# Kernel optimization log

Hardware: AMD Instinct MI355X
Metric: run time of the kernel (lower is better)

## Reference

```python
import jax, jax.numpy as jnp
import numpy as np

HEADS = 4
DIM_QK = 128
DIM_V = 128
FMAP = 32  # H = W = 32, L = 1024
DIM = 512
B = 16


def rel_to_abs(x):
    # x: [B, Nh, L, 2L-1] -> [B, Nh, L, L]
    b, nh, L, _ = x.shape
    x = jnp.pad(x, ((0, 0), (0, 0), (0, 0), (0, 1)))          # [B, Nh, L, 2L]
    flat = x.reshape(b, nh, L * 2 * L)
    flat = jnp.pad(flat, ((0, 0), (0, 0), (0, L - 1)))
    final = flat.reshape(b, nh, L + 1, 2 * L - 1)
    return final[:, :, :L, L - 1:]


def relative_logits_1d(q, rel_k):
    # q: [B, Nh, H, W, d], rel_k: [2W-1, d] -> [B, Nh, H, H, W, W]
    b, nh, h, w, _ = q.shape
    rl = jnp.einsum('bnhwd,md->bnhwm', q, rel_k)
    rl = rl.reshape(b, nh * h, w, 2 * w - 1)
    rl = rel_to_abs(rl)                                        # [B, Nh*H, W, W]
    rl = rl.reshape(b, nh, h, w, w)
    rl = jnp.broadcast_to(rl[:, :, :, None], (b, nh, h, h, w, w))
    return rl


def rel_pos_logits(q, rel_height, rel_width):
    # q: [B, Nh, L, d] with L = FMAP*FMAP -> [B, Nh, L, L]
    b, nh, L, d = q.shape
    h = w = FMAP
    q5 = q.reshape(b, nh, h, w, d)
    # width logits: 'b n x i y j -> b n (x y) (i j)'
    rw = relative_logits_1d(q5, rel_width)
    rw = rw.transpose(0, 1, 2, 4, 3, 5).reshape(b, nh, h * w, h * w)
    # height logits: transpose spatial, then 'b n x i y j -> b n (y x) (j i)'
    rh = relative_logits_1d(q5.transpose(0, 1, 3, 2, 4), rel_height)
    rh = rh.transpose(0, 1, 4, 2, 5, 3).reshape(b, nh, h * w, h * w)
    return rw + rh


def setup_inputs() -> dict:
    key = jax.random.key(0)
    k1, k2, k3, k4, k5 = jax.random.split(key, 5)
    scale = DIM_QK ** -0.5
    return {
        'featuremap': jax.random.normal(k1, (B, DIM, FMAP, FMAP), jnp.float32),
        'w_qk': jax.random.normal(k2, (2 * HEADS * DIM_QK, DIM), jnp.float32) * (DIM ** -0.5),
        'w_v': jax.random.normal(k3, (HEADS * DIM_V, DIM), jnp.float32) * (DIM ** -0.5),
        'rel_height': jax.random.normal(k4, (2 * FMAP - 1, DIM_QK), jnp.float32) * scale,
        'rel_width': jax.random.normal(k5, (2 * FMAP - 1, DIM_QK), jnp.float32) * scale,
    }


def reference(featuremap, w_qk, w_v, rel_height, rel_width):
    b, c, h, w = featuremap.shape
    L = h * w
    # 1x1 convs (no bias) == channel matmuls
    qk = jnp.einsum('bchw,oc->bohw', featuremap, w_qk)
    q, k = jnp.split(qk, 2, axis=1)
    v = jnp.einsum('bchw,oc->bohw', featuremap, w_v)

    def to_heads(x, d):
        # 'B (h d) H W -> B h (H W) d'
        return x.reshape(b, HEADS, d, L).transpose(0, 1, 3, 2)

    q = to_heads(q, DIM_QK) * (DIM_QK ** -0.5)
    k = to_heads(k, DIM_QK)
    v = to_heads(v, DIM_V)

    logits = jnp.einsum('bhxd,bhyd->bhxy', q, k)
    logits = logits + rel_pos_logits(q, rel_height, rel_width)
    weights = jax.nn.softmax(logits, axis=-1)
    attn = jnp.einsum('bhxy,bhyd->bhxd', weights, v)
    # 'B h (H W) d -> B (h d) H W'
    out = attn.transpose(0, 1, 3, 2).reshape(b, HEADS * DIM_V, h, w)
    return out
```

## Files before the change

### kernel.cpp

```cpp
#include <hip/hip_runtime.h>
#include <hip/hip_bf16.h>
#include <math.h>

typedef __bf16 bf16x8 __attribute__((ext_vector_type(8)));
typedef float f32x4 __attribute__((ext_vector_type(4)));

#define QSCALE_L2E (0.08838834764831845f * 1.4426950408889634f)

static __device__ __forceinline__ unsigned short bits_bf16(float v) {
  __hip_bfloat16 h = __float2bfloat16(v);
  return *reinterpret_cast<unsigned short*>(&h);
}

static __device__ __forceinline__ void gload16(const void* g, void* l) {
  __builtin_amdgcn_global_load_lds(
      (const __attribute__((address_space(1))) void*)g,
      (__attribute__((address_space(3))) void*)l, 16, 0, 0);
}

__global__ __launch_bounds__(256) void k_convw(const float* __restrict__ wqk,
                                               const float* __restrict__ wv,
                                               const float* __restrict__ relw,
                                               const float* __restrict__ relh,
                                               __hip_bfloat16* __restrict__ wall,
                                               __hip_bfloat16* __restrict__ relsb) {
  int i = blockIdx.x * 256 + threadIdx.x;
  if (i < 1536 * 512) {
    float v = (i < 1024 * 512) ? wqk[i] : wv[i - 1024 * 512];
    wall[i] = __float2bfloat16(v);
  } else {
    int j = i - 1536 * 512;
    int t = j >> 13, m = (j >> 7) & 63, d = j & 127;
    float v = (m < 63) ? (t ? relh[m * 128 + d] : relw[m * 128 + d]) : 0.f;
    relsb[j] = __float2bfloat16(v);
  }
}

__global__ __launch_bounds__(256) void k_tfm(const float* __restrict__ fm,
                                             __hip_bfloat16* __restrict__ fmt) {
  __shared__ float t[64][65];
  int lt = blockIdx.x, ct = blockIdx.y, b = blockIdx.z;
  int tid = threadIdx.x;
  const float* src = fm + ((size_t)b * 512 + ct * 64) * 1024 + lt * 64;
#pragma unroll
  for (int i = 0; i < 16; ++i) {
    int idx = i * 256 + tid;
    int r = idx >> 6, cl = idx & 63;
    t[r][cl] = src[(size_t)r * 1024 + cl];
  }
  __syncthreads();
  __hip_bfloat16* dst = fmt + ((size_t)b * 1024 + lt * 64) * 512 + ct * 64;
#pragma unroll
  for (int i = 0; i < 16; ++i) {
    int idx = i * 256 + tid;
    int r = idx >> 6, cc = idx & 63;
    dst[(size_t)r * 512 + cc] = __float2bfloat16(t[cc][r]);
  }
}

__global__ __launch_bounds__(256) void k_gemm(const __hip_bfloat16* __restrict__ fmt,
                                              const __hip_bfloat16* __restrict__ wall,
                                              __hip_bfloat16* __restrict__ Qb,
                                              __hip_bfloat16* __restrict__ Kb,
                                              __hip_bfloat16* __restrict__ Vt) {
  __shared__ char smem[32768];
  char* As = smem;
  char* Bs = smem + 16384;
  int bm = blockIdx.x, bn = blockIdx.y, b = blockIdx.z;
  int tid = threadIdx.x;
  int lane = tid & 63, wave = tid >> 6;
  int wr = wave >> 1, wc = wave & 1;
  int g = lane >> 4, ln = lane & 15;
  const char* Ag = (const char*)(fmt + ((size_t)b * 1024 + bm * 128) * 512);
  const char* Bg = (const char*)(wall + (size_t)bn * 128 * 512);

  int j3 = lane >> 3, j7 = lane & 7;
  int segsrc = ((j7 ^ j3) << 4);

  f32x4 acc[4][4] = {};
  for (int kb = 0; kb < 8; ++kb) {
#pragma unroll
    for (int i = 0; i < 4; ++i) {
      int R = (wave * 4 + i) * 8;
      size_t go = (size_t)(R + j3) * 1024 + (size_t)kb * 128 + segsrc;
      gload16(Ag + go, As + R * 128);
      gload16(Bg + go, Bs + R * 128);
    }
    __syncthreads();
#pragma unroll
    for (int ks = 0; ks < 2; ++ks) {
      int kcol = ks * 64 + (g << 4);
      bf16x8 af[4], bfr[4];
#pragma unroll
      for (int m = 0; m < 4; ++m) {
        int row = wr * 64 + m * 16 + ln;
        af[m] = *(const bf16x8*)(As + row * 128 + (kcol ^ ((ln & 7) << 4)));
      }
#pragma unroll
      for (int n = 0; n < 4; ++n) {
        int row = wc * 64 + n * 16 + ln;
        bfr[n] = *(const bf16x8*)(Bs + row * 128 + (kcol ^ ((ln & 7) << 4)));
      }
#pragma unroll
      for (int m = 0; m < 4; ++m)
#pragma unroll
        for (int n = 0; n < 4; ++n)
          acc[m][n] = __builtin_amdgcn_mfma_f32_16x16x32_bf16(af[m], bfr[n], acc[m][n], 0, 0, 0);
    }
    __syncthreads();
  }

  int otype = bn >> 2;
  int head = bn & 3;
  if (otype != 2) {
    float sc = (otype == 0) ? QSCALE_L2E : 1.0f;
#pragma unroll
    for (int m = 0; m < 4; ++m)
#pragma unroll
      for (int n = 0; n < 4; ++n) {
        int d = wc * 64 + n * 16 + ln;
#pragma unroll
        for (int r = 0; r < 4; ++r) {
          int l = wr * 64 + m * 16 + g * 4 + r;
          *(__hip_bfloat16*)(smem + l * 256 + ((d * 2) ^ ((l & 7) << 4))) =
              __float2bfloat16(acc[m][n][r] * sc);
        }
      }
    __syncthreads();
    __hip_bfloat16* dstb =
        (otype == 0 ? Qb : Kb) + (((size_t)(b * 4 + head) * 1024) + bm * 128) * 128;
#pragma unroll
    for (int i = 0; i < 8; ++i) {
      int idx = i * 256 + tid;
      int row = idx >> 4, c16 = idx & 15;
      uint4 v = *(const uint4*)(smem + row * 256 + ((c16 * 16) ^ ((row & 7) << 4)));
      *(uint4*)(dstb + (size_t)row * 128 + c16 * 8) = v;
    }
  } else {
#pragma unroll
    for (int m = 0; m < 4; ++m)
#pragma unroll
      for (int n = 0; n < 4; ++n) {
        int d = wc * 64 + n * 16 + ln;
        int lbase = wr * 64 + m * 16 + g * 4;
        ushort4 pk;
        pk.x = bits_bf16(acc[m][n][0]);
        pk.y = bits_bf16(acc[m][n][1]);
        pk.z = bits_bf16(acc[m][n][2]);
        pk.w = bits_bf16(acc[m][n][3]);
        *(ushort4*)(smem + d * 256 + ((lbase * 2) ^ ((d & 7) << 4))) = pk;
      }
    __syncthreads();
    __hip_bfloat16* dstb = Vt + ((size_t)(b * 4 + head) * 128) * 1024 + bm * 128;
#pragma unroll
    for (int i = 0; i < 8; ++i) {
      int idx = i * 256 + tid;
      int row = idx >> 4, c16 = idx & 15;
      uint4 v = *(const uint4*)(smem + row * 256 + ((c16 * 16) ^ ((row & 7) << 4)));
      *(uint4*)(dstb + (size_t)row * 1024 + c16 * 8) = v;
    }
  }
}

__global__ __launch_bounds__(256) void k_bias(const __hip_bfloat16* __restrict__ Qb,
                                              const __hip_bfloat16* __restrict__ relsb,
                                              float* __restrict__ QRW,
                                              float* __restrict__ QRH) {
  __shared__ char sh[32768];
  int bx = blockIdx.x, bh = blockIdx.y;
  int tid = threadIdx.x, lane = tid & 63, wave = tid >> 6;
  int g = lane >> 4, ln = lane & 15;
#pragma unroll
  for (int i = 0; i < 8; ++i) {
    int chunk = i * 256 + tid;
    int row = chunk >> 4, c16 = chunk & 15;
    *(uint4*)(sh + row * 256 + ((c16 * 16) ^ ((row & 7) << 4))) =
        *(const uint4*)(relsb + (size_t)row * 128 + c16 * 8);
  }
  __syncthreads();
  size_t bhL = (size_t)bh * 1024;
  int l0 = bx * 128 + wave * 32;
  const __hip_bfloat16* Qg = Qb + (bhL + l0) * 128;
  bf16x8 a[2][4];
#pragma unroll
  for (int lf = 0; lf < 2; ++lf)
#pragma unroll
    for (int ks = 0; ks < 4; ++ks)
      a[lf][ks] = *(const bf16x8*)(Qg + (size_t)(lf * 16 + ln) * 128 + ks * 32 + g * 8);
#pragma unroll
  for (int t = 0; t < 2; ++t) {
    float* dst = (t == 0 ? QRW : QRH) + (bhL + l0) * 64;
#pragma unroll
    for (int n = 0; n < 4; ++n) {
      f32x4 acc2[2] = {};
#pragma unroll
      for (int ks = 0; ks < 4; ++ks) {
        int mrow = n * 16 + ln;
        bf16x8 bf = *(const bf16x8*)(sh + t * 16384 + mrow * 256 +
                                     ((ks * 64 + g * 16) ^ ((mrow & 7) << 4)));
#pragma unroll
        for (int lf = 0; lf < 2; ++lf)
          acc2[lf] = __builtin_amdgcn_mfma_f32_16x16x32_bf16(a[lf][ks], bf, acc2[lf], 0, 0, 0);
      }
#pragma unroll
      for (int lf = 0; lf < 2; ++lf)
#pragma unroll
        for (int r = 0; r < 4; ++r)
          dst[(size_t)(lf * 16 + g * 4 + r) * 64 + n * 16 + ln] = acc2[lf][r];
    }
  }
}

__global__ __launch_bounds__(512, 2) void k_attn(const __hip_bfloat16* __restrict__ Qb,
                                                 const __hip_bfloat16* __restrict__ Kb,
                                                 const __hip_bfloat16* __restrict__ Vt,
                                                 const float* __restrict__ QRW,
                                                 const float* __restrict__ QRH,
                                                 float* __restrict__ out) {
  extern __shared__ char smem[];
  float* hb_s = (float*)smem;
  char* kbuf = smem + 40960;
  char* vbuf = smem + 40960 + 32768;
  char* pt = smem + 40960 + 65536;

  int bh = blockIdx.x, qt = blockIdx.y;
  int b = bh >> 2, h = bh & 3;
  int tid = threadIdx.x, lane = tid & 63, wave = tid >> 6;
  int g = lane >> 4, ln = lane & 15;
  int q0 = qt * 256;
  size_t bhL = (size_t)bh * 1024;

#pragma unroll
  for (int i = 0; i < 5; ++i) {
    int c = i * 512 + tid;
    if (c < 2304) {
      int row = c / 9, j = c % 9;
      int s0 = (31 - ((q0 + row) >> 5)) & ~3;
      *(uint4*)(hb_s + row * 40 + j * 4) =
          *(const uint4*)(QRH + (bhL + q0 + row) * 64 + s0 + j * 4);
    }
  }

  bf16x8 qa[2][4];
  float wb[2][2][4];
  int qloc[2], hbase[2];
#pragma unroll
  for (int u = 0; u < 2; ++u) {
    qloc[u] = wave * 32 + u * 16 + ln;
    int qg = q0 + qloc[u];
    int cx = qg & 31, rx = qg >> 5;
    hbase[u] = (31 - rx) & 3;
    const __hip_bfloat16* qrow = Qb + (bhL + qg) * 128;
#pragma unroll
    for (int ks = 0; ks < 4; ++ks)
      qa[u][ks] = *(const bf16x8*)(qrow + ks * 32 + g * 8);
    const float* wrow = QRW + (bhL + qg) * 64 + (31 - cx) + g * 4;
#pragma unroll
    for (int half = 0; half < 2; ++half)
#pragma unroll
      for (int r = 0; r < 4; ++r) wb[u][half][r] = wrow[half * 16 + r];
  }

  const char* Kg0 = (const char*)(Kb + bhL * 128);
  const char* Vg0 = (const char*)(Vt + (size_t)bh * 128 * 1024);
  int j3 = lane >> 3, j7 = lane & 7;
  int segv = ((j7 ^ j3) << 4);

  auto STAGE = [&](int bsel, int kt2) {
    const char* Kg = Kg0 + (size_t)kt2 * 64 * 256;
    char* kvb = kbuf + bsel * 16384;
#pragma unroll
    for (int i = 0; i < 2; ++i) {
      int R = (wave * 2 + i) * 4;
      int seg = ((lane & 15) ^ ((i & 1) * 4 + (lane >> 4))) << 4;
      gload16(Kg + (size_t)(R + (lane >> 4)) * 256 + seg, kvb + R * 256);
    }
    const char* Vg = Vg0 + (size_t)kt2 * 128;
    char* vtb = vbuf + bsel * 16384;
#pragma unroll
    for (int i = 0; i < 2; ++i) {
      int R = (wave * 2 + i) * 8;
      gload16(Vg + (size_t)(R + j3) * 2048 + segv, vtb + R * 128);
    }
  };

  f32x4 acc[2][8] = {};
  float mrow[2] = {-1e30f, -1e30f}, lrow[2] = {0.f, 0.f};
  char* pw = pt + wave * 4096;

  STAGE(0, 0);
  __syncthreads();

  for (int kt = 0; kt < 16; ++kt) {
    int cur = kt & 1;
    if (kt < 15) STAGE(cur ^ 1, kt + 1);
    char* kvb = kbuf + cur * 16384;
    char* vtb = vbuf + cur * 16384;

    f32x4 s[2][4] = {};
    __builtin_amdgcn_s_setprio(1);
#pragma unroll
    for (int ks = 0; ks < 4; ++ks) {
      int kcol = ks * 64 + (g << 4);
#pragma unroll
      for (int n = 0; n < 4; ++n) {
        int krow = n * 16 + ln;
        bf16x8 kf = *(const bf16x8*)(kvb + krow * 256 + (kcol ^ ((krow & 7) << 4)));
        s[0][n] = __builtin_amdgcn_mfma_f32_16x16x32_bf16(kf, qa[0][ks], s[0][n], 0, 0, 0);
        s[1][n] = __builtin_amdgcn_mfma_f32_16x16x32_bf16(kf, qa[1][ks], s[1][n], 0, 0, 0);
      }
    }
    __builtin_amdgcn_s_setprio(0);
#pragma unroll
    for (int u = 0; u < 2; ++u) {
      float hb0 = hb_s[qloc[u] * 40 + hbase[u] + kt * 2];
      float hb1 = hb_s[qloc[u] * 40 + hbase[u] + kt * 2 + 1];
#pragma unroll
      for (int n = 0; n < 4; ++n) {
        float hb = (n >> 1) ? hb1 : hb0;
#pragma unroll
        for (int r = 0; r < 4; ++r) s[u][n][r] += wb[u][n & 1][r] + hb;
      }
      float mt = s[u][0][0];
#pragma unroll
      for (int n = 0; n < 4; ++n)
#pragma unroll
        for (int r = 0; r < 4; ++r) mt = fmaxf(mt, s[u][n][r]);
      mt = fmaxf(mt, __shfl_xor(mt, 16, 64));
      mt = fmaxf(mt, __shfl_xor(mt, 32, 64));
      float mn = fmaxf(mrow[u], mt);
      float alpha = exp2f(mrow[u] - mn);
      mrow[u] = mn;
      float rs = 0.f;
#pragma unroll
      for (int n = 0; n < 4; ++n)
#pragma unroll
        for (int r = 0; r < 4; ++r) {
          s[u][n][r] = exp2f(s[u][n][r] - mn);
          rs += s[u][n][r];
        }
      rs += __shfl_xor(rs, 16, 64);
      rs += __shfl_xor(rs, 32, 64);
      lrow[u] = lrow[u] * alpha + rs;
#pragma unroll
      for (int mf = 0; mf < 8; ++mf) acc[u][mf] *= alpha;
#pragma unroll
      for (int n = 0; n < 4; ++n) {
        ushort4 pk;
        pk.x = bits_bf16(s[u][n][0]);
        pk.y = bits_bf16(s[u][n][1]);
        pk.z = bits_bf16(s[u][n][2]);
        pk.w = bits_bf16(s[u][n][3]);
        *(ushort4*)(pw + (u * 16 + ln) * 128 + ((n * 32 + g * 8) ^ ((ln & 7) << 4))) = pk;
      }
    }
    __builtin_amdgcn_s_setprio(1);
#pragma unroll
    for (int ks2 = 0; ks2 < 2; ++ks2) {
      int kcb = ks2 * 64 + (g << 4);
      bf16x8 pb0 = *(const bf16x8*)(pw + ln * 128 + (kcb ^ ((ln & 7) << 4)));
      bf16x8 pb1 = *(const bf16x8*)(pw + (16 + ln) * 128 + (kcb ^ ((ln & 7) << 4)));
#pragma unroll
      for (int mf = 0; mf < 8; ++mf) {
        int vrow = mf * 16 + ln;
        bf16x8 av = *(const bf16x8*)(vtb + vrow * 128 + (kcb ^ ((vrow & 7) << 4)));
        acc[0][mf] = __builtin_amdgcn_mfma_f32_16x16x32_bf16(av, pb0, acc[0][mf], 0, 0, 0);
        acc[1][mf] = __builtin_amdgcn_mfma_f32_16x16x32_bf16(av, pb1, acc[1][mf], 0, 0, 0);
      }
    }
    __builtin_amdgcn_s_setprio(0);
    __syncthreads();
  }
#pragma unroll
  for (int u = 0; u < 2; ++u) {
    float linv = 1.0f / lrow[u];
    int qg3 = q0 + wave * 32 + u * 16 + ln;
#pragma unroll
    for (int mf = 0; mf < 8; ++mf) {
      int dbase = mf * 16 + g * 4;
#pragma unroll
      for (int r = 0; r < 4; ++r) {
        out[((size_t)(b * 512 + h * 128 + dbase + r)) * 1024 + qg3] = acc[u][mf][r] * linv;
      }
    }
  }
}

extern "C" void kernel_launch(void* const* d_in, const int* in_sizes, int n_in,
                              void* d_out, int out_size, void* d_ws, size_t ws_size,
                              hipStream_t stream) {
  const float* fm = (const float*)d_in[0];
  const float* wqk = (const float*)d_in[1];
  const float* wv = (const float*)d_in[2];
  const float* relh = (const float*)d_in[3];
  const float* relw = (const float*)d_in[4];
  float* out = (float*)d_out;
  char* w = (char*)d_ws;

  __hip_bfloat16* fmt = (__hip_bfloat16*)w;
  __hip_bfloat16* wall = (__hip_bfloat16*)(w + 16777216);
  __hip_bfloat16* Qb = (__hip_bfloat16*)(w + 18350080);
  __hip_bfloat16* Kb = (__hip_bfloat16*)(w + 35127296);
  __hip_bfloat16* Vt = (__hip_bfloat16*)(w + 51904512);
  float* QRW = (float*)(w + 68681728);
  float* QRH = (float*)(w + 85458944);
  __hip_bfloat16* relsb = (__hip_bfloat16*)(w + 102236160);

  hipFuncSetAttribute((const void*)k_attn,
                      hipFuncAttributeMaxDynamicSharedMemorySize, 139264);

  k_convw<<<3136, 256, 0, stream>>>(wqk, wv, relw, relh, wall, relsb);
  k_tfm<<<dim3(16, 8, 16), 256, 0, stream>>>(fm, fmt);
  k_gemm<<<dim3(8, 12, 16), 256, 0, stream>>>(fmt, wall, Qb, Kb, Vt);
  k_bias<<<dim3(8, 64), 256, 0, stream>>>(Qb, relsb, QRW, QRH);
  k_attn<<<dim3(64, 4), 512, 139264, stream>>>(Qb, Kb, Vt, QRW, QRH, out);
}
```

Measured before the change: 125.4 us.

## Software-pipeline QK^T of next tile with softmax/PV of previous tile in attention

Restructures the flash-attention loop so that tile kt's QK^T MFMAs are issued before the softmax and PV of tile kt-1. A triple-buffered V ring and double-buffered score registers support this, letting MFMA work overlap the exp/reduction work. It also adds a lazy rescale that only updates the running max when it grows by more than 8 (log2 units), which skips alpha multiplies on the accumulators. The cost is more LDS (grows to 152KB) and more registers, which could hurt occupancy, plus a relaxed max bound that slightly risks overflow or precision issues.

```diff
diff --git a/kernel.cpp b/kernel.cpp
--- a/kernel.cpp
+++ b/kernel.cpp
@@ -219,9 +219,12 @@
                                                  float* __restrict__ out) {
   extern __shared__ char smem[];
   float* hb_s = (float*)smem;
-  char* kbuf = smem + 40960;
-  char* vbuf = smem + 40960 + 32768;
-  char* pt = smem + 40960 + 65536;
+  char* kb0 = smem + 40960;
+  char* kb1 = smem + 57344;
+  char* vb0 = smem + 73728;
+  char* vb1 = smem + 90112;
+  char* vb2 = smem + 106496;
+  char* pt = smem + 122880;
 
   int bh = blockIdx.x, qt = blockIdx.y;
   int b = bh >> 2, h = bh & 3;
@@ -266,17 +269,17 @@
   int j3 = lane >> 3, j7 = lane & 7;
   int segv = ((j7 ^ j3) << 4);
 
-  auto STAGE = [&](int bsel, int kt2) {
+  auto STAGE_K = [&](char* kvb, int kt2) {
     const char* Kg = Kg0 + (size_t)kt2 * 64 * 256;
-    char* kvb = kbuf + bsel * 16384;
 #pragma unroll
     for (int i = 0; i < 2; ++i) {
       int R = (wave * 2 + i) * 4;
       int seg = ((lane & 15) ^ ((i & 1) * 4 + (lane >> 4))) << 4;
       gload16(Kg + (size_t)(R + (lane >> 4)) * 256 + seg, kvb + R * 256);
     }
+  };
+  auto STAGE_V = [&](char* vtb, int kt2) {
     const char* Vg = Vg0 + (size_t)kt2 * 128;
-    char* vtb = vbuf + bsel * 16384;
 #pragma unroll
     for (int i = 0; i < 2; ++i) {
       int R = (wave * 2 + i) * 8;
@@ -288,71 +291,58 @@
   float mrow[2] = {-1e30f, -1e30f}, lrow[2] = {0.f, 0.f};
   char* pw = pt + wave * 4096;
 
-  STAGE(0, 0);
-  __syncthreads();
-
-  for (int kt = 0; kt < 16; ++kt) {
-    int cur = kt & 1;
-    if (kt < 15) STAGE(cur ^ 1, kt + 1);
-    char* kvb = kbuf + cur * 16384;
-    char* vtb = vbuf + cur * 16384;
-
-    f32x4 s[2][4] = {};
-    __builtin_amdgcn_s_setprio(1);
-#pragma unroll
-    for (int ks = 0; ks < 4; ++ks) {
-      int kcol = ks * 64 + (g << 4);
-#pragma unroll
-      for (int n = 0; n < 4; ++n) {
-        int krow = n * 16 + ln;
-        bf16x8 kf = *(const bf16x8*)(kvb + krow * 256 + (kcol ^ ((krow & 7) << 4)));
-        s[0][n] = __builtin_amdgcn_mfma_f32_16x16x32_bf16(kf, qa[0][ks], s[0][n], 0, 0, 0);
-        s[1][n] = __builtin_amdgcn_mfma_f32_16x16x32_bf16(kf, qa[1][ks], s[1][n], 0, 0, 0);
-      }
-    }
-    __builtin_amdgcn_s_setprio(0);
+  auto SMPV = [&](int kp, f32x4 (&sO)[2][4], char* vprev) {
+    float mt[2];
 #pragma unroll
     for (int u = 0; u < 2; ++u) {
-      float hb0 = hb_s[qloc[u] * 40 + hbase[u] + kt * 2];
-      float hb1 = hb_s[qloc[u] * 40 + hbase[u] + kt * 2 + 1];
+      float hb0 = hb_s[qloc[u] * 40 + hbase[u] + kp * 2];
+      float hb1 = hb_s[qloc[u] * 40 + hbase[u] + kp * 2 + 1];
 #pragma unroll
       for (int n = 0; n < 4; ++n) {
         float hb = (n >> 1) ? hb1 : hb0;
 #pragma unroll
-        for (int r = 0; r < 4; ++r) s[u][n][r] += wb[u][n & 1][r] + hb;
-      }
-      float mt = s[u][0][0];
+        for (int r = 0; r < 4; ++r) sO[u][n][r] += wb[u][n & 1][r] + hb;
+      }
+      float m = sO[u][0][0];
 #pragma unroll
       for (int n = 0; n < 4; ++n)
 #pragma unroll
-        for (int r = 0; r < 4; ++r) mt = fmaxf(mt, s[u][n][r]);
-      mt = fmaxf(mt, __shfl_xor(mt, 16, 64));
-      mt = fmaxf(mt, __shfl_xor(mt, 32, 64));
-      float mn = fmaxf(mrow[u], mt);
-      float alpha = exp2f(mrow[u] - mn);
-      mrow[u] = mn;
+        for (int r = 0; r < 4; ++r) m = fmaxf(m, sO[u][n][r]);
+      m = fmaxf(m, __shfl_xor(m, 16, 64));
+      mt[u] = fmaxf(m, __shfl_xor(m, 32, 64));
+    }
+    bool grow = (mt[0] > mrow[0] + 8.f) || (mt[1] > mrow[1] + 8.f);
+    if (__any(grow)) {
+#pragma unroll
+      for (int u = 0; u < 2; ++u) {
+        float mn = fmaxf(mrow[u], mt[u]);
+        float alpha = exp2f(mrow[u] - mn);
+        mrow[u] = mn;
+        lrow[u] *= alpha;
+#pragma unroll
+        for (int mf = 0; mf < 8; ++mf) acc[u][mf] *= alpha;
+      }
+    }
+#pragma unroll
+    for (int u = 0; u < 2; ++u) {
       float rs = 0.f;
 #pragma unroll
-      for (int n = 0; n < 4; ++n)
+      for (int n = 0; n < 4; ++n) {
 #pragma unroll
         for (int r = 0; r < 4; ++r) {
-          s[u][n][r] = exp2f(s[u][n][r] - mn);
-          rs += s[u][n][r];
+          sO[u][n][r] = exp2f(sO[u][n][r] - mrow[u]);
+          rs += sO[u][n][r];
         }
+        ushort4 pk;
+        pk.x = bits_bf16(sO[u][n][0]);
+        pk.y = bits_bf16(sO[u][n][1]);
+        pk.z = bits_bf16(sO[u][n][2]);
+        pk.w = bits_bf16(sO[u][n][3]);
+        *(ushort4*)(pw + (u * 16 + ln) * 128 + ((n * 32 + g * 8) ^ ((ln & 7) << 4))) = pk;
+      }
       rs += __shfl_xor(rs, 16, 64);
       rs += __shfl_xor(rs, 32, 64);
-      lrow[u] = lrow[u] * alpha + rs;
-#pragma unroll
-      for (int mf = 0; mf < 8; ++mf) acc[u][mf] *= alpha;
-#pragma unroll
-      for (int n = 0; n < 4; ++n) {
-        ushort4 pk;
-        pk.x = bits_bf16(s[u][n][0]);
-        pk.y = bits_bf16(s[u][n][1]);
-        pk.z = bits_bf16(s[u][n][2]);
-        pk.w = bits_bf16(s[u][n][3]);
-        *(ushort4*)(pw + (u * 16 + ln) * 128 + ((n * 32 + g * 8) ^ ((ln & 7) << 4))) = pk;
-      }
+      lrow[u] += rs;
     }
     __builtin_amdgcn_s_setprio(1);
 #pragma unroll
@@ -363,14 +353,58 @@
 #pragma unroll
       for (int mf = 0; mf < 8; ++mf) {
         int vrow = mf * 16 + ln;
-        bf16x8 av = *(const bf16x8*)(vtb + vrow * 128 + (kcb ^ ((vrow & 7) << 4)));
+        bf16x8 av = *(const bf16x8*)(vprev + vrow * 128 + (kcb ^ ((vrow & 7) << 4)));
         acc[0][mf] = __builtin_amdgcn_mfma_f32_16x16x32_bf16(av, pb0, acc[0][mf], 0, 0, 0);
         acc[1][mf] = __builtin_amdgcn_mfma_f32_16x16x32_bf16(av, pb1, acc[1][mf], 0, 0, 0);
       }
     }
     __builtin_amdgcn_s_setprio(0);
+  };
+
+  char *kc = kb0, *kn = kb1;
+  char *vp = vb2, *vc = vb0, *vn = vb1;
+
+  STAGE_K(kc, 0);
+  STAGE_V(vc, 0);
+  __syncthreads();
+
+  f32x4 sA[2][4], sB[2][4];
+
+  auto body = [&](int kt, f32x4 (&sN)[2][4], f32x4 (&sO)[2][4]) {
+    if (kt < 15) {
+      STAGE_K(kn, kt + 1);
+      STAGE_V(vn, kt + 1);
+    }
+#pragma unroll
+    for (int n = 0; n < 4; ++n) {
+      sN[0][n] = (f32x4){0.f, 0.f, 0.f, 0.f};
+      sN[1][n] = (f32x4){0.f, 0.f, 0.f, 0.f};
+    }
+    __builtin_amdgcn_s_setprio(1);
+#pragma unroll
+    for (int ks = 0; ks < 4; ++ks) {
+      int kcol = ks * 64 + (g << 4);
+#pragma unroll
+      for (int n = 0; n < 4; ++n) {
+        int krow = n * 16 + ln;
+        bf16x8 kf = *(const bf16x8*)(kc + krow * 256 + (kcol ^ ((krow & 7) << 4)));
+        sN[0][n] = __builtin_amdgcn_mfma_f32_16x16x32_bf16(kf, qa[0][ks], sN[0][n], 0, 0, 0);
+        sN[1][n] = __builtin_amdgcn_mfma_f32_16x16x32_bf16(kf, qa[1][ks], sN[1][n], 0, 0, 0);
+      }
+    }
+    __builtin_amdgcn_s_setprio(0);
+    if (kt > 0) SMPV(kt - 1, sO, vp);
     __syncthreads();
-  }
+    char* t = kc; kc = kn; kn = t;
+    char* t2 = vp; vp = vc; vc = vn; vn = t2;
+  };
+
+  for (int kt = 0; kt < 16; kt += 2) {
+    body(kt, sA, sB);
+    body(kt + 1, sB, sA);
+  }
+  SMPV(15, sB, vp);
+
 #pragma unroll
   for (int u = 0; u < 2; ++u) {
     float linv = 1.0f / lrow[u];
@@ -407,11 +441,11 @@
   __hip_bfloat16* relsb = (__hip_bfloat16*)(w + 102236160);
 
   hipFuncSetAttribute((const void*)k_attn,
-                      hipFuncAttributeMaxDynamicSharedMemorySize, 139264);
+                      hipFuncAttributeMaxDynamicSharedMemorySize, 155648);
 
   k_convw<<<3136, 256, 0, stream>>>(wqk, wv, relw, relh, wall, relsb);
   k_tfm<<<dim3(16, 8, 16), 256, 0, stream>>>(fm, fmt);
   k_gemm<<<dim3(8, 12, 16), 256, 0, stream>>>(fmt, wall, Qb, Kb, Vt);
   k_bias<<<dim3(8, 64), 256, 0, stream>>>(Qb, relsb, QRW, QRH);
-  k_attn<<<dim3(64, 4), 512, 139264, stream>>>(Qb, Kb, Vt, QRW, QRH, out);
-}
+  k_attn<<<dim3(64, 4), 512, 155648, stream>>>(Qb, Kb, Vt, QRW, QRH, out);
+}
```

After: 120.9 us. 1.04x faster.
